# Performance work log

Hardware: AMD Instinct MI355X
Metric: run time of the kernel (lower is better)

## Reference

```python
import jax, jax.numpy as jnp
import numpy as np
from jax import lax

NFFT, WIN, HOP = 512, 320, 160
PAD = NFFT // 2
F = NFFT // 2 + 1  # 257

def _window():
    # torch.hann_window(320, periodic=True), center-padded to n_fft=512 (torch.stft convention)
    w = 0.5 - 0.5 * jnp.cos(2.0 * jnp.pi * jnp.arange(WIN, dtype=jnp.float32) / WIN)
    lp = (NFFT - WIN) // 2
    return jnp.pad(w, (lp, NFFT - WIN - lp))

def _stft(x):  # [N, L] -> [N, T, F] complex64 (center=True, reflect pad)
    xp = jnp.pad(x, ((0, 0), (PAD, PAD)), mode='reflect')
    T = 1 + (xp.shape[1] - NFFT) // HOP
    idx = jnp.arange(T)[:, None] * HOP + jnp.arange(NFFT)[None, :]
    frames = xp[:, idx] * _window()  # [N, T, NFFT]
    return jnp.fft.rfft(frames, axis=-1)

def _istft(spec, length):  # [N, T, F] complex -> [N, length]
    win = _window()
    frames = jnp.fft.irfft(spec, n=NFFT, axis=-1) * win  # [N, T, NFFT]
    N, T, _ = frames.shape
    total = (T - 1) * HOP + NFFT
    pos = (jnp.arange(T)[:, None] * HOP + jnp.arange(NFFT)[None, :]).reshape(-1)
    out = jnp.zeros((N, total), frames.dtype).at[:, pos].add(frames.reshape(N, -1))
    wsq = jnp.zeros((total,), win.dtype).at[pos].add(jnp.tile(win * win, T))
    out = out / jnp.maximum(wsq, 1e-11)[None, :]
    return out[:, PAD:PAD + length]

def _lstm(x, W_ih, W_hh, b_ih, b_hh):  # x [N, T, D] -> [N, T, H]
    N, T, _ = x.shape
    H = W_hh.shape[1]
    xW = x @ W_ih.T + (b_ih + b_hh)  # precompute input projections [N, T, 4H]
    def step(carry, xt):
        h, c = carry
        g = xt + h @ W_hh.T
        i, f, gg, o = jnp.split(g, 4, axis=-1)  # torch gate order i,f,g,o
        c = jax.nn.sigmoid(f) * c + jax.nn.sigmoid(i) * jnp.tanh(gg)
        h = jax.nn.sigmoid(o) * jnp.tanh(c)
        return (h, c), h
    h0 = jnp.zeros((N, H), x.dtype)
    _, hs = lax.scan(step, (h0, h0), jnp.swapaxes(xW, 0, 1))
    return jnp.swapaxes(hs, 0, 1)

def _forward(x, W_ih, W_hh, b_ih, b_hh, W1, b1, W2, b2):
    B, L, C = x.shape
    xm = jnp.transpose(x, (0, 2, 1)).reshape(B * C, L)
    spec = _stft(xm).reshape(B, C, -1, F)  # [B, C, T, F] == r_spec + 1j*i_spec
    T = spec.shape[2]
    feat = jnp.concatenate([spec.real, spec.imag], axis=-1).reshape(B * C, T, 2 * F)
    h = _lstm(feat, W_ih, W_hh, b_ih, b_hh)  # [B*C, T, 128]
    def masked(Wl, bl):
        m = h @ Wl.T + bl                      # [B*C, T, 514]
        rm, im = jnp.split(m, 2, axis=-1)
        mask = (rm + 1j * im).reshape(B, C, T, F)
        return mask * spec                      # complex mask multiply
    s_spec = masked(W1, b1)
    n_spec = masked(W2, b2)
    # per-frequency PSD matrices over time
    psd_s = jnp.einsum('bctf,betf->bfce', s_spec, jnp.conj(s_spec)) / T
    psd_n = jnp.einsum('bctf,betf->bfce', n_spec, jnp.conj(n_spec)) / T
    tr_n = jnp.einsum('bfcc->bf', psd_n).real
    eye = jnp.eye(C, dtype=psd_n.dtype)
    psd_n = psd_n + (1e-6 * tr_n / C + 1e-8)[..., None, None] * eye  # diagonal loading
    num = jnp.linalg.solve(psd_n, psd_s)                             # [B, F, C, C]
    ws = num / (jnp.einsum('bfcc->bf', num)[..., None, None] + 1e-8)
    w = ws[..., 0]                                                   # ref_channel = 0 -> [B, F, C]
    obs = jnp.transpose(spec, (0, 3, 1, 2))                          # [B, F, C, T]
    enh = jnp.einsum('bfc,bfct->bft', jnp.conj(w), obs)              # beamformed [B, F, T]
    return _istft(jnp.transpose(enh, (0, 2, 1)), L)                  # [B, L]

def setup_inputs() -> dict:
    key = jax.random.key(0)
    ks = jax.random.split(key, 8)
    D, H = 2 * F, 128
    s = 0.05
    return {
        'x': jax.random.normal(ks[0], (8, 96000, 8), jnp.float32),
        'W_ih': jax.random.normal(ks[1], (4 * H, D), jnp.float32) * s,
        'W_hh': jax.random.normal(ks[2], (4 * H, H), jnp.float32) * s,
        'b_ih': jnp.zeros((4 * H,), jnp.float32),
        'b_hh': jnp.zeros((4 * H,), jnp.float32),
        'W1': jax.random.normal(ks[3], (D, H), jnp.float32) * s,
        'b1': jnp.zeros((D,), jnp.float32),
        'W2': jax.random.normal(ks[4], (D, H), jnp.float32) * s,
        'b2': jnp.zeros((D,), jnp.float32),
    }

def reference(x, W_ih, W_hh, b_ih, b_hh, W1, b1, W2, b2):
    return _forward(x, W_ih, W_hh, b_ih, b_hh, W1, b1, W2, b2)
```

## Files before the change

### kernel.cpp

```cpp
#include <hip/hip_runtime.h>
#include <math.h>

#define NFFT  512
#define WINL  320
#define HOP   160
#define FPAD  256
#define NF    257
#define TT    601
#define LSEQ  96000
#define XPLEN 96512
#define NCH   8
#define NB    8
#define NSEQ  64
#define NROWS 38464
#define DD    514
#define HH    128
#define G4    512
#define KPAD  544
#define NCOMB 1026

#define NXP   24128
#define NWSQ  377
#define NBFF  1028
#define NWT   1088
#define NBI   1088
#define NBS   2
#define NWM   640
#define NWP   128
#define NINIT (NXP + NWSQ + NBFF + NWT + NBI + NBS + NWM + NWP)

typedef _Float16 h2v __attribute__((ext_vector_type(2)));
typedef short bf16x8 __attribute__((ext_vector_type(8)));
typedef float f32x4 __attribute__((ext_vector_type(4)));

__device__ __forceinline__ float winval(int k) {
  if (k < 96 || k >= 416) return 0.f;
  return 0.5f - 0.5f * cosf((float)(2.0 * M_PI / 320.0) * (float)(k - 96));
}

__device__ __forceinline__ void split_bf16(float v, unsigned short* h, unsigned short* l) {
  unsigned int hb = __float_as_uint(v) >> 16;
  float r = v - __uint_as_float(hb << 16);
  *h = (unsigned short)hb;
  *l = (unsigned short)(__float_as_uint(r) >> 16);
}

__device__ __forceinline__ void glds16(const unsigned short* g, unsigned short* l) {
  __builtin_amdgcn_global_load_lds(
      (const __attribute__((address_space(1))) void*)g,
      (__attribute__((address_space(3))) void*)l,
      16, 0, 0);
}

__device__ __forceinline__ int xcd_swz(int orig, int nwg) {
  int q = nwg >> 3, r = nwg & 7;
  int xcd = orig & 7, slot = orig >> 3;
  return (xcd < r ? xcd * (q + 1) : r * (q + 1) + (xcd - r) * q) + slot;
}

__global__ void k_init(const float* __restrict__ x, const float* __restrict__ Wih,
                       const float* __restrict__ Whh, const float* __restrict__ bih,
                       const float* __restrict__ bhh, const float* __restrict__ W1,
                       const float* __restrict__ W2,
                       unsigned short* __restrict__ XPh, unsigned short* __restrict__ XPl,
                       float* __restrict__ wsq, float* __restrict__ BFf,
                       unsigned short* __restrict__ WTh, unsigned short* __restrict__ WTl,
                       unsigned short* __restrict__ BIh, unsigned short* __restrict__ BIl,
                       float* __restrict__ BSUM,
                       unsigned short* __restrict__ W1h, unsigned short* __restrict__ W1l,
                       unsigned short* __restrict__ W2h, unsigned short* __restrict__ W2l,
                       unsigned int* __restrict__ WhhP4) {
  int b = blockIdx.x;
  const int tid = threadIdx.x;

  if (b < NXP) {
    int idx = b * 256 + tid;
    if (idx < NSEQ * XPLEN) {
      int n = idx / XPLEN, i = idx - n * XPLEN;
      int j = i - FPAD;
      if (j < 0) j = -j;
      else if (j >= LSEQ) j = 2 * LSEQ - 2 - j;
      int bb = n >> 3, c = n & 7;
      float v = x[((long)bb * LSEQ + j) * NCH + c];
      split_bf16(v, &XPh[idx], &XPl[idx]);
    }
    return;
  }
  b -= NXP;

  if (b < NWSQ) {
    int p = b * 256 + tid;
    if (p < XPLEN) {
      int t0 = (p <= 511) ? 0 : (p - 352) / 160;
      int t1 = p / 160; if (t1 > 600) t1 = 600;
      float s = 0.f;
      for (int t = t0; t <= t1; t++) { float w = winval(p - t * HOP); s += w * w; }
      wsq[p] = s;
    }
    return;
  }
  b -= NWSQ;

  if (b < NBFF) {
    int idx = b * 256 + tid;
    if (idx < NFFT * DD) {
      int k = idx / DD, d = idx - k * DD;
      float w = winval(k);
      int f = (d < NF) ? d : d - NF;
      int m = (k * f) & 511;
      float th = (float)(M_PI / 256.0) * (float)m;
      BFf[idx] = ((d < NF) ? cosf(th) : -sinf(th)) * w;
    }
    return;
  }
  b -= NBFF;

  if (b < NWT) {
    int idx = b * 256 + tid;
    if (idx < G4 * KPAD) {
      int n = idx / KPAD, k = idx - n * KPAD;
      float v = (k < DD) ? Wih[n * DD + k] : 0.f;
      split_bf16(v, &WTh[idx], &WTl[idx]);
    }
    return;
  }
  b -= NWT;

  if (b < NBI) {
    int idx = b * 256 + tid;
    if (idx < NFFT * KPAD) {
      int n = idx / KPAD, kk = idx - n * KPAD;
      float v = 0.f;
      if (kk < DD) {
        float w = winval(n);
        int f = (kk < NF) ? kk : kk - NF;
        int edge = (f == 0 || f == 256);
        float alpha = edge ? 1.f : 2.f;
        int m = (n * f) & 511;
        float th = (float)(M_PI / 256.0) * (float)m;
        float c;
        if (kk < NF) c = alpha * cosf(th);
        else         c = edge ? 0.f : -alpha * sinf(th);
        v = c * w * (1.f / 512.f);
      }
      split_bf16(v, &BIh[idx], &BIl[idx]);
    }
    return;
  }
  b -= NBI;

  if (b < NBS) {
    int idx = b * 256 + tid;
    if (idx < G4) BSUM[idx] = bih[idx] + bhh[idx];
    return;
  }
  b -= NBS;

  if (b < NWM) {
    int idx = b * 256 + tid;
    if (idx < 2 * 640 * HH) {
      int m = idx / (640 * HH);
      int rem = idx - m * 640 * HH;
      int np = rem / HH, k = rem - np * HH;
      int ri = np / 320, f = np - ri * 320;
      float v = 0.f;
      if (f < NF) {
        int fcol = (ri == 0) ? f : NF + f;
        v = (m == 0) ? W1[fcol * HH + k] : W2[fcol * HH + k];
      }
      unsigned short h, l;
      split_bf16(v, &h, &l);
      if (m == 0) { W1h[rem] = h; W1l[rem] = l; }
      else        { W2h[rem] = h; W2l[rem] = l; }
    }
    return;
  }
  b -= NWM;

  {
    int idx = b * 256 + tid;
    if (idx < G4 * 64) {
      int j = idx >> 6, k2 = idx & 63;
      _Float16 lo = (_Float16)Whh[j * HH + 2 * k2];
      _Float16 hi = (_Float16)Whh[j * HH + 2 * k2 + 1];
      unsigned int u = ((unsigned int)__builtin_bit_cast(unsigned short, hi) << 16)
                     |  (unsigned int)__builtin_bit_cast(unsigned short, lo);
      WhhP4[(k2 >> 2) * (G4 * 4) + j * 4 + (k2 & 3)] = u;
    }
  }
}

__global__ void k_bcomb(const float* __restrict__ BWf, unsigned short* __restrict__ H,
                        unsigned short* __restrict__ L) {
  int idx = blockIdx.x * 256 + threadIdx.x;
  if (idx >= 1152 * KPAD) return;
  int n = idx / KPAD, k = idx - n * KPAD;
  float v = 0.f;
  if (k < NFFT) {
    if (n < DD) {
      float w = winval(k);
      int f = (n < NF) ? n : n - NF;
      int m = (k * f) & 511;
      float th = (float)(M_PI / 256.0) * (float)m;
      v = ((n < NF) ? cosf(th) : -sinf(th)) * w;
    } else if (n < NCOMB) {
      v = BWf[k * G4 + (n - 514)];
    }
  }
  split_bf16(v, &H[idx], &L[idx]);
}

template <int GATHER>
__launch_bounds__(256)
__global__ void k_gemm3(const float* __restrict__ A,
                        const unsigned short* __restrict__ Bth,
                        const unsigned short* __restrict__ Btl,
                        const float* __restrict__ bias, float* __restrict__ C,
                        int M, int N, int K, int lda, int ldc) {
  __shared__ __align__(16) unsigned short sAh[128 * 40];
  __shared__ __align__(16) unsigned short sAl[128 * 40];
  __shared__ __align__(16) unsigned short sBh[128 * 40];
  __shared__ __align__(16) unsigned short sBl[128 * 40];
  const int tid = threadIdx.x;
  const int row0 = blockIdx.y * 128, col0 = blockIdx.x * 128;
  const int sar = tid >> 1, sak = (tid & 1) * 16;
  const int arow = row0 + sar;
  long abase = (long)arow * lda;
  const bool arok = (arow < M);
  const int lane = tid & 63, w = tid >> 6;
  const int wm = (w >> 1) * 64, wn = (w & 1) * 64;
  const int l15 = lane & 15, quad = lane >> 4;
  f32x4 acc[4][4] = {};
  unsigned int* aH = (unsigned int*)sAh;
  unsigned int* aL = (unsigned int*)sAl;
  uint4* bH = (uint4*)sBh;
  uint4* bL = (uint4*)sBl;
  for (int k0 = 0; k0 < K; k0 += 32) {
#pragma unroll
    for (int i = 0; i < 8; i++) {
      int kk = k0 + sak + 2 * i;
      float v0 = 0.f, v1 = 0.f;
      if (arok) {
        if (kk + 1 < K) { float2 t2 = *(const float2*)(A + abase + kk); v0 = t2.x; v1 = t2.y; }
        else if (kk < K) { v0 = A[abase + kk]; }
      }
      unsigned int h0 = __float_as_uint(v0) >> 16, h1 = __float_as_uint(v1) >> 16;
      float r0 = v0 - __uint_as_float(h0 << 16), r1 = v1 - __uint_as_float(h1 << 16);
      unsigned int l0 = __float_as_uint(r0) >> 16, l1 = __float_as_uint(r1) >> 16;
      aH[sar * 20 + (sak >> 1) + i] = h0 | (h1 << 16);
      aL[sar * 20 + (sak >> 1) + i] = l0 | (l1 << 16);
    }
#pragma unroll
    for (int h = 0; h < 2; h++) {
      int idx = tid + h * 256;
      int r = idx >> 2, c = idx & 3;
      long go = (long)(col0 + r) * KPAD + k0 + c * 8;
      bH[r * 5 + c] = *(const uint4*)(Bth + go);
      bL[r * 5 + c] = *(const uint4*)(Btl + go);
    }
    __syncthreads();
    bf16x8 ah[4], al[4], bh[4], bl[4];
#pragma unroll
    for (int i = 0; i < 4; i++) {
      int off = (wm + i * 16 + l15) * 40 + quad * 8;
      ah[i] = *(const bf16x8*)(sAh + off);
      al[i] = *(const bf16x8*)(sAl + off);
      int boff = (wn + i * 16 + l15) * 40 + quad * 8;
      bh[i] = *(const bf16x8*)(sBh + boff);
      bl[i] = *(const bf16x8*)(sBl + boff);
    }
#pragma unroll
    for (int i = 0; i < 4; i++)
#pragma unroll
      for (int j = 0; j < 4; j++) {
        acc[i][j] = __builtin_amdgcn_mfma_f32_16x16x32_bf16(al[i], bh[j], acc[i][j], 0, 0, 0);
        acc[i][j] = __builtin_amdgcn_mfma_f32_16x16x32_bf16(ah[i], bl[j], acc[i][j], 0, 0, 0);
        acc[i][j] = __builtin_amdgcn_mfma_f32_16x16x32_bf16(ah[i], bh[j], acc[i][j], 0, 0, 0);
      }
    __syncthreads();
  }
#pragma unroll
  for (int i = 0; i < 4; i++)
#pragma unroll
    for (int j = 0; j < 4; j++) {
      int cc = col0 + wn + j * 16 + l15;
      if (cc >= N) continue;
      float bv = bias ? bias[cc] : 0.f;
#pragma unroll
      for (int rg = 0; rg < 4; rg++) {
        int rr = row0 + wm + i * 16 + quad * 4 + rg;
        if (rr < M) C[(long)rr * ldc + cc] = acc[i][j][rg] + bv;
      }
    }
}

__launch_bounds__(256)
__global__ void k_gemm4(const unsigned short* __restrict__ Ah, const unsigned short* __restrict__ Al,
                        const unsigned short* __restrict__ Bh, const unsigned short* __restrict__ Bl,
                        const float* __restrict__ bsum, float* __restrict__ S,
                        float* __restrict__ XW) {
  __shared__ __align__(16) unsigned short sAh[128 * 32];
  __shared__ __align__(16) unsigned short sAl[128 * 32];
  __shared__ __align__(16) unsigned short sBh[128 * 32];
  __shared__ __align__(16) unsigned short sBl[128 * 32];
  const int tid = threadIdx.x;
  const int wg = xcd_swz(blockIdx.x, 9 * 301);
  const int row0 = (wg / 9) * 128, col0 = (wg % 9) * 128;
  const int lane = tid & 63, w = tid >> 6;
  const int wm = (w >> 1) * 64, wn = (w & 1) * 64;
  const int l15 = lane & 15, quad = lane >> 4;
  const int sr0 = w * 32 + (lane >> 2);
  const int sr1 = sr0 + 16;
  const int c8 = (lane & 3) * 8;
  long ab0, ab1;
  { int rr = row0 + sr0; int n = rr / TT, t = rr - n * TT; ab0 = (long)n * XPLEN + (long)t * HOP + c8; }
  { int rr = row0 + sr1; int n = rr / TT, t = rr - n * TT; ab1 = (long)n * XPLEN + (long)t * HOP + c8; }
  const long bb0 = (long)(col0 + sr0) * KPAD + c8;
  const long bb1 = (long)(col0 + sr1) * KPAD + c8;
  const int d0 = w * 1024;
  const int d1 = d0 + 512;
  f32x4 acc[4][4] = {};
  for (int k0 = 0; k0 < NFFT; k0 += 32) {
    glds16(Ah + ab0 + k0, sAh + d0);
    glds16(Ah + ab1 + k0, sAh + d1);
    glds16(Al + ab0 + k0, sAl + d0);
    glds16(Al + ab1 + k0, sAl + d1);
    glds16(Bh + bb0 + k0, sBh + d0);
    glds16(Bh + bb1 + k0, sBh + d1);
    glds16(Bl + bb0 + k0, sBl + d0);
    glds16(Bl + bb1 + k0, sBl + d1);
    __syncthreads();
    bf16x8 ah[4], al[4], bh[4], bl[4];
#pragma unroll
    for (int i = 0; i < 4; i++) {
      int off = (wm + i * 16 + l15) * 32 + quad * 8;
      ah[i] = *(const bf16x8*)(sAh + off);
      al[i] = *(const bf16x8*)(sAl + off);
      int boff = (wn + i * 16 + l15) * 32 + quad * 8;
      bh[i] = *(const bf16x8*)(sBh + boff);
      bl[i] = *(const bf16x8*)(sBl + boff);
    }
#pragma unroll
    for (int i = 0; i < 4; i++)
#pragma unroll
      for (int j = 0; j < 4; j++) {
        acc[i][j] = __builtin_amdgcn_mfma_f32_16x16x32_bf16(al[i], bh[j], acc[i][j], 0, 0, 0);
        acc[i][j] = __builtin_amdgcn_mfma_f32_16x16x32_bf16(ah[i], bl[j], acc[i][j], 0, 0, 0);
        acc[i][j] = __builtin_amdgcn_mfma_f32_16x16x32_bf16(ah[i], bh[j], acc[i][j], 0, 0, 0);
      }
    __syncthreads();
  }
#pragma unroll
  for (int i = 0; i < 4; i++)
#pragma unroll
    for (int j = 0; j < 4; j++) {
      int cc = col0 + wn + j * 16 + l15;
      if (cc >= NCOMB) continue;
#pragma unroll
      for (int rg = 0; rg < 4; rg++) {
        int rr = row0 + wm + i * 16 + quad * 4 + rg;
        if (rr >= NROWS) continue;
        float v = acc[i][j][rg];
        if (cc < DD) S[(long)rr * DD + cc] = v;
        else         XW[(long)rr * G4 + (cc - 514)] = v + bsum[cc - 514];
      }
    }
}

__launch_bounds__(256)
__global__ void k_gemm5(const unsigned short* __restrict__ Ah, const unsigned short* __restrict__ Al,
                        const unsigned short* __restrict__ Bh, const unsigned short* __restrict__ Bl,
                        float* __restrict__ C, int M, int N, int ldc) {
  __shared__ __align__(16) unsigned short sAh[128 * 40];
  __shared__ __align__(16) unsigned short sAl[128 * 40];
  __shared__ __align__(16) unsigned short sBh[128 * 40];
  __shared__ __align__(16) unsigned short sBl[128 * 40];
  const int tid = threadIdx.x;
  const int row0 = blockIdx.y * 128, col0 = blockIdx.x * 128;
  const int sr0 = tid >> 2, c4 = (tid & 3) * 8, cq = tid & 3;
  const int lane = tid & 63, w = tid >> 6;
  const int wm = (w >> 1) * 64, wn = (w & 1) * 64;
  const int l15 = lane & 15, quad = lane >> 4;
  f32x4 acc[4][4] = {};
  uint4* aH4 = (uint4*)sAh; uint4* aL4 = (uint4*)sAl;
  uint4* bH4 = (uint4*)sBh; uint4* bL4 = (uint4*)sBl;
  for (int k0 = 0; k0 < KPAD; k0 += 32) {
    {
      long go = (long)(row0 + sr0) * KPAD + k0 + c4;
      aH4[sr0 * 5 + cq] = *(const uint4*)(Ah + go);
      aL4[sr0 * 5 + cq] = *(const uint4*)(Al + go);
      go = (long)(row0 + sr0 + 64) * KPAD + k0 + c4;
      aH4[(sr0 + 64) * 5 + cq] = *(const uint4*)(Ah + go);
      aL4[(sr0 + 64) * 5 + cq] = *(const uint4*)(Al + go);
    }
    {
      long go = (long)(col0 + sr0) * KPAD + k0 + c4;
      bH4[sr0 * 5 + cq] = *(const uint4*)(Bh + go);
      bL4[sr0 * 5 + cq] = *(const uint4*)(Bl + go);
      go = (long)(col0 + sr0 + 64) * KPAD + k0 + c4;
      bH4[(sr0 + 64) * 5 + cq] = *(const uint4*)(Bh + go);
      bL4[(sr0 + 64) * 5 + cq] = *(const uint4*)(Bl + go);
    }
    __syncthreads();
    bf16x8 ah[4], al[4], bh[4], bl[4];
#pragma unroll
    for (int i = 0; i < 4; i++) {
      int off = (wm + i * 16 + l15) * 40 + quad * 8;
      ah[i] = *(const bf16x8*)(sAh + off);
      al[i] = *(const bf16x8*)(sAl + off);
      int boff = (wn + i * 16 + l15) * 40 + quad * 8;
      bh[i] = *(const bf16x8*)(sBh + boff);
      bl[i] = *(const bf16x8*)(sBl + boff);
    }
#pragma unroll
    for (int i = 0; i < 4; i++)
#pragma unroll
      for (int j = 0; j < 4; j++) {
        acc[i][j] = __builtin_amdgcn_mfma_f32_16x16x32_bf16(al[i], bh[j], acc[i][j], 0, 0, 0);
        acc[i][j] = __builtin_amdgcn_mfma_f32_16x16x32_bf16(ah[i], bl[j], acc[i][j], 0, 0, 0);
        acc[i][j] = __builtin_amdgcn_mfma_f32_16x16x32_bf16(ah[i], bh[j], acc[i][j], 0, 0, 0);
      }
    __syncthreads();
  }
#pragma unroll
  for (int i = 0; i < 4; i++)
#pragma unroll
    for (int j = 0; j < 4; j++) {
      int cc = col0 + wn + j * 16 + l15;
      if (cc >= N) continue;
#pragma unroll
      for (int rg = 0; rg < 4; rg++) {
        int rr = row0 + wm + i * 16 + quad * 4 + rg;
        if (rr < M) C[(long)rr * ldc + cc] = acc[i][j][rg];
      }
    }
}

__device__ __forceinline__ float tanh_fast(float x) {
  float e = __expf(2.f * x);
  return 1.f - 2.f / (e + 1.f);
}

__launch_bounds__(512, 2)
__global__ void k_lstm(const float* __restrict__ XW, const unsigned int* __restrict__ WhhP4,
                       float* __restrict__ Hout) {
  __shared__ __align__(16) unsigned int hl2[64];
  __shared__ float gl[G4];
  const int j = threadIdx.x;
  const int n = blockIdx.x;
  const uint4* W4 = (const uint4*)WhhP4;
  unsigned int wp[64];
#pragma unroll
  for (int i4 = 0; i4 < 16; i4++) {
    uint4 v = W4[i4 * G4 + j];
    wp[4 * i4]     = v.x;
    wp[4 * i4 + 1] = v.y;
    wp[4 * i4 + 2] = v.z;
    wp[4 * i4 + 3] = v.w;
  }
  float cst = 0.f;
  if (j < 64) hl2[j] = 0u;
  const float* xwrow = XW + (long)n * TT * G4 + j;
  float xnext = xwrow[0];
  const uint4* h4 = (const uint4*)hl2;
  const bool isg = (j >= 2 * HH) && (j < 3 * HH);
  __syncthreads();
  for (int t = 0; t < TT; t++) {
    float xv = xnext;
    if (t + 1 < TT) xnext = xwrow[(long)(t + 1) * G4];
    float a0 = 0.f, a1 = 0.f, a2 = 0.f, a3 = 0.f;
#pragma unroll
    for (int k = 0; k < 16; k++) {
      uint4 hv4 = h4[k];
      a0 = __builtin_amdgcn_fdot2(__builtin_bit_cast(h2v, hv4.x), __builtin_bit_cast(h2v, wp[4 * k]),     a0, false);
      a1 = __builtin_amdgcn_fdot2(__builtin_bit_cast(h2v, hv4.y), __builtin_bit_cast(h2v, wp[4 * k + 1]), a1, false);
      a2 = __builtin_amdgcn_fdot2(__builtin_bit_cast(h2v, hv4.z), __builtin_bit_cast(h2v, wp[4 * k + 2]), a2, false);
      a3 = __builtin_amdgcn_fdot2(__builtin_bit_cast(h2v, hv4.w), __builtin_bit_cast(h2v, wp[4 * k + 3]), a3, false);
    }
    float a = ((a0 + a1) + (a2 + a3)) + xv;
    float nl;
    if (isg) nl = tanh_fast(a);
    else     nl = 1.f / (1.f + __expf(-a));
    gl[j] = nl;
    asm volatile("s_waitcnt lgkmcnt(0)" ::: "memory");
    __builtin_amdgcn_s_barrier();
    if (j < HH) {
      float ni = gl[j], nf = gl[HH + j], ng = gl[2 * HH + j], no = gl[3 * HH + j];
      cst = nf * cst + ni * ng;
      float hv = no * tanh_fast(cst);
      ((_Float16*)hl2)[j] = (_Float16)hv;
      Hout[((long)n * TT + t) * HH + j] = hv;
    }
    asm volatile("s_waitcnt lgkmcnt(0)" ::: "memory");
    __builtin_amdgcn_s_barrier();
  }
}

__launch_bounds__(256)
__global__ void k_maskms(const float* __restrict__ Hout,
                         const unsigned short* __restrict__ Wsh,
                         const unsigned short* __restrict__ Wsl,
                         const float* __restrict__ bias, const float* __restrict__ S,
                         float* __restrict__ MS) {
  __shared__ __align__(16) unsigned short sAh[64 * 40];
  __shared__ __align__(16) unsigned short sAl[64 * 40];
  __shared__ __align__(16) unsigned short sBh[64 * 40];
  __shared__ __align__(16) unsigned short sBl[64 * 40];
  __shared__ float Cs[64][68];
  __shared__ float SR[64][33];
  __shared__ float SI[64][33];
  const int tid = threadIdx.x;
  const int wg = xcd_swz(blockIdx.x, 9 * 601);
  const int f0 = (wg % 9) * 32;
  const int row0 = (wg / 9) * 64;
  const int lane = tid & 63, w = tid >> 6;
  const int wm = w * 16;
  const int l15 = lane & 15, quad = lane >> 4;
  const int sar = tid >> 2;
  const int sak = (tid & 3) * 8;
  const int np = ((sar < 32) ? 0 : 320 - 32) + f0 + sar;
  unsigned int* aH = (unsigned int*)sAh;
  unsigned int* aL = (unsigned int*)sAl;
  f32x4 acc[4] = {};
  for (int k0 = 0; k0 < HH; k0 += 32) {
    {
      const float* ap = Hout + (long)(row0 + sar) * HH + k0 + sak;
      float4 v0 = *(const float4*)ap;
      float4 v1 = *(const float4*)(ap + 4);
      float vv[8] = {v0.x, v0.y, v0.z, v0.w, v1.x, v1.y, v1.z, v1.w};
#pragma unroll
      for (int i = 0; i < 4; i++) {
        unsigned int h0 = __float_as_uint(vv[2 * i]) >> 16, h1 = __float_as_uint(vv[2 * i + 1]) >> 16;
        float r0 = vv[2 * i] - __uint_as_float(h0 << 16), r1 = vv[2 * i + 1] - __uint_as_float(h1 << 16);
        unsigned int l0 = __float_as_uint(r0) >> 16, l1 = __float_as_uint(r1) >> 16;
        aH[sar * 20 + (sak >> 1) + i] = h0 | (h1 << 16);
        aL[sar * 20 + (sak >> 1) + i] = l0 | (l1 << 16);
      }
    }
    {
      long go = (long)np * HH + k0 + sak;
      *(uint4*)(sBh + sar * 40 + sak) = *(const uint4*)(Wsh + go);
      *(uint4*)(sBl + sar * 40 + sak) = *(const uint4*)(Wsl + go);
    }
    __syncthreads();
    bf16x8 ah = *(const bf16x8*)(sAh + (wm + l15) * 40 + quad * 8);
    bf16x8 al = *(const bf16x8*)(sAl + (wm + l15) * 40 + quad * 8);
#pragma unroll
    for (int ct = 0; ct < 4; ct++) {
      bf16x8 bh = *(const bf16x8*)(sBh + (ct * 16 + l15) * 40 + quad * 8);
      bf16x8 bl = *(const bf16x8*)(sBl + (ct * 16 + l15) * 40 + quad * 8);
      acc[ct] = __builtin_amdgcn_mfma_f32_16x16x32_bf16(al, bh, acc[ct], 0, 0, 0);
      acc[ct] = __builtin_amdgcn_mfma_f32_16x16x32_bf16(ah, bl, acc[ct], 0, 0, 0);
      acc[ct] = __builtin_amdgcn_mfma_f32_16x16x32_bf16(ah, bh, acc[ct], 0, 0, 0);
    }
    __syncthreads();
  }
#pragma unroll
  for (int ct = 0; ct < 4; ct++) {
    int col = ct * 16 + l15;
    int f = f0 + (col & 31);
    int fcol = (col < 32) ? f : NF + f;
    float bv = (f < NF) ? bias[fcol] : 0.f;
#pragma unroll
    for (int rg = 0; rg < 4; rg++) Cs[wm + quad * 4 + rg][col] = acc[ct][rg] + bv;
  }
  __syncthreads();
  {
    int fl = tid & 31, r8 = tid >> 5;
    int f = f0 + fl;
#pragma unroll
    for (int i = 0; i < 8; i++) {
      int rl = r8 * 8 + i;
      int rr = row0 + rl;
      float rm = Cs[rl][fl], im = Cs[rl][32 + fl];
      float sr = 0.f, si = 0.f;
      if (f < NF) { sr = S[(long)rr * DD + f]; si = S[(long)rr * DD + NF + f]; }
      SR[rl][fl] = rm * sr - im * si;
      SI[rl][fl] = rm * si + im * sr;
    }
  }
  __syncthreads();
  {
    int tl = tid & 63, fq = tid >> 6;
    int rr = row0 + tl;
    int n = rr / TT, t = rr - n * TT;
    int b = n >> 3, c = n & 7;
#pragma unroll
    for (int i = 0; i < 8; i++) {
      int fl = fq * 8 + i;
      int f = f0 + fl;
      if (f < NF) {
        long addr = ((((long)b * NF + f) * 8 + c) * (long)TT + t) * 2;
        *(float2*)&MS[addr] = make_float2(SR[tl][fl], SI[tl][fl]);
      }
    }
  }
}

__launch_bounds__(256)
__global__ void k_psd(const float* __restrict__ MS, float* __restrict__ PSD) {
  __shared__ float buf[9616];
  __shared__ float part[64][8];
  const int tid = threadIdx.x;
  const long base = (long)blockIdx.x * 9616;
  for (int i = tid; i < 9616; i += 256) buf[i] = MS[base + i];
  __syncthreads();
  int p = tid & 63, q = tid >> 6;
  int c = p >> 3, e = p & 7;
  const float2* xc = (const float2*)&buf[c * 1202];
  const float2* xe = (const float2*)&buf[e * 1202];
  int t0 = q * 150, t1 = (q == 3) ? TT : t0 + 150;
  float ar = 0.f, ai = 0.f;
  for (int t = t0; t < t1; t++) {
    float2 m = xc[t];
    float2 v = xe[t];
    ar += m.x * v.x + m.y * v.y;
    ai += m.y * v.x - m.x * v.y;
  }
  part[p][q * 2] = ar; part[p][q * 2 + 1] = ai;
  __syncthreads();
  if (tid < 64) {
    float sr = part[tid][0] + part[tid][2] + part[tid][4] + part[tid][6];
    float si = part[tid][1] + part[tid][3] + part[tid][5] + part[tid][7];
    PSD[((long)blockIdx.x * 64 + tid) * 2]     = sr * (1.f / 601.f);
    PSD[((long)blockIdx.x * 64 + tid) * 2 + 1] = si * (1.f / 601.f);
  }
}

__launch_bounds__(64)
__global__ void k_solve(const float* __restrict__ PS, const float* __restrict__ PN,
                        float* __restrict__ WV) {
  int idx = blockIdx.x * 64 + threadIdx.x;
  if (idx >= NB * NF) return;
  float Ar[8][8], Ai[8][8], Br[8][8], Bi[8][8];
  const float* pn = PN + (long)idx * 128;
  const float* ps = PS + (long)idx * 128;
  for (int i = 0; i < 8; i++)
    for (int j = 0; j < 8; j++) {
      Ar[i][j] = pn[(i * 8 + j) * 2]; Ai[i][j] = pn[(i * 8 + j) * 2 + 1];
      Br[i][j] = ps[(i * 8 + j) * 2]; Bi[i][j] = ps[(i * 8 + j) * 2 + 1];
    }
  float tr = 0.f;
  for (int i = 0; i < 8; i++) tr += Ar[i][i];
  float load = 1e-6f * tr / 8.f + 1e-8f;
  for (int i = 0; i < 8; i++) Ar[i][i] += load;
  for (int k = 0; k < 8; k++) {
    int piv = k; float mx = Ar[k][k] * Ar[k][k] + Ai[k][k] * Ai[k][k];
    for (int i = k + 1; i < 8; i++) {
      float m2 = Ar[i][k] * Ar[i][k] + Ai[i][k] * Ai[i][k];
      if (m2 > mx) { mx = m2; piv = i; }
    }
    if (piv != k) {
      for (int j = 0; j < 8; j++) {
        float t0;
        t0 = Ar[k][j]; Ar[k][j] = Ar[piv][j]; Ar[piv][j] = t0;
        t0 = Ai[k][j]; Ai[k][j] = Ai[piv][j]; Ai[piv][j] = t0;
        t0 = Br[k][j]; Br[k][j] = Br[piv][j]; Br[piv][j] = t0;
        t0 = Bi[k][j]; Bi[k][j] = Bi[piv][j]; Bi[piv][j] = t0;
      }
    }
    float dr = Ar[k][k], di = Ai[k][k];
    float inv = 1.f / (dr * dr + di * di);
    float irr = dr * inv, iii = -di * inv;
    for (int j = 0; j < 8; j++) {
      float xr = Ar[k][j], xi = Ai[k][j];
      Ar[k][j] = xr * irr - xi * iii; Ai[k][j] = xr * iii + xi * irr;
      xr = Br[k][j]; xi = Bi[k][j];
      Br[k][j] = xr * irr - xi * iii; Bi[k][j] = xr * iii + xi * irr;
    }
    for (int i = 0; i < 8; i++) {
      if (i == k) continue;
      float fr = Ar[i][k], fi = Ai[i][k];
      for (int j = 0; j < 8; j++) {
        float kr = Ar[k][j], ki = Ai[k][j];
        Ar[i][j] -= fr * kr - fi * ki;
        Ai[i][j] -= fr * ki + fi * kr;
        kr = Br[k][j]; ki = Bi[k][j];
        Br[i][j] -= fr * kr - fi * ki;
        Bi[i][j] -= fr * ki + fi * kr;
      }
    }
  }
  float trr = 1e-8f, tri = 0.f;
  for (int i = 0; i < 8; i++) { trr += Br[i][i]; tri += Bi[i][i]; }
  float inv = 1.f / (trr * trr + tri * tri);
  for (int c = 0; c < 8; c++) {
    float xr = Br[c][0], xi = Bi[c][0];
    WV[((long)idx * 8 + c) * 2]     = (xr * trr + xi * tri) * inv;
    WV[((long)idx * 8 + c) * 2 + 1] = (xi * trr - xr * tri) * inv;
  }
}

__launch_bounds__(320)
__global__ void k_beam(const float* __restrict__ S, const float* __restrict__ WV,
                       unsigned short* __restrict__ ENHh, unsigned short* __restrict__ ENHl) {
  __shared__ float WL[NF * 16];
  int bb = blockIdx.x / TT, t = blockIdx.x - bb * TT;
  for (int i = threadIdx.x; i < NF * 16; i += 320) WL[i] = WV[(long)bb * NF * 16 + i];
  __syncthreads();
  int f = threadIdx.x;
  long base = ((long)bb * TT + t) * KPAD;
  if (f < NF) {
    float er = 0.f, ei = 0.f;
#pragma unroll
    for (int c = 0; c < 8; c++) {
      float wr = WL[(f * 8 + c) * 2], wi = WL[(f * 8 + c) * 2 + 1];
      const float* srow = S + (((long)(bb * 8 + c) * TT) + t) * DD;
      float sr = srow[f], si = srow[NF + f];
      er += wr * sr + wi * si;
      ei += wr * si - wi * sr;
    }
    split_bf16(er, &ENHh[base + f], &ENHl[base + f]);
    split_bf16(ei, &ENHh[base + NF + f], &ENHl[base + NF + f]);
  }
  int z = threadIdx.x - 288;
  if (z >= 0 && z < 30) { ENHh[base + DD + z] = 0; ENHl[base + DD + z] = 0; }
}

__global__ void k_ola(const float* __restrict__ IFR, const float* __restrict__ WSQ,
                      float* __restrict__ out) {
  int idx = blockIdx.x * 256 + threadIdx.x;
  if (idx >= NB * LSEQ) return;
  int b = idx / LSEQ, l = idx - b * LSEQ;
  int p = l + FPAD;
  int t0 = (p <= 511) ? 0 : (p - 352) / 160;
  int t1 = p / 160; if (t1 > 600) t1 = 600;
  float s = 0.f;
  for (int t = t0; t <= t1; t++) s += IFR[((long)b * TT + t) * NFFT + (p - t * HOP)];
  out[idx] = s / fmaxf(WSQ[p], 1e-11f);
}

extern "C" void kernel_launch(void* const* d_in, const int* in_sizes, int n_in,
                              void* d_out, int out_size, void* d_ws, size_t ws_size,
                              hipStream_t stream) {
  (void)in_sizes; (void)n_in; (void)out_size; (void)ws_size;
  const float* x   = (const float*)d_in[0];
  const float* Wih = (const float*)d_in[1];
  const float* Whh = (const float*)d_in[2];
  const float* bih = (const float*)d_in[3];
  const float* bhh = (const float*)d_in[4];
  const float* W1  = (const float*)d_in[5];
  const float* b1  = (const float*)d_in[6];
  const float* W2  = (const float*)d_in[7];
  const float* b2  = (const float*)d_in[8];
  float* ws = (float*)d_ws;

  unsigned short* XPh = (unsigned short*)(ws + 0);
  unsigned short* XPl = (unsigned short*)(ws + 3088384);
  float* S     = ws + 6176768;
  float* XWM   = ws + 25951264;
  float* HOUT  = ws + 45725760;
  float* PSD_S = ws + 50650048;
  float* PSD_N = ws + 50913216;
  float* WV    = ws + 51176384;
  float* BSUM  = ws + 51209280;
  float* WSQ   = ws + 51209792;
  unsigned short* W1sh = (unsigned short*)(ws + 51306304);
  unsigned short* W1sl = (unsigned short*)(ws + 51347264);
  unsigned short* W2sh = (unsigned short*)(ws + 51388224);
  unsigned short* W2sl = (unsigned short*)(ws + 51429184);
  unsigned short* WTth = (unsigned short*)(ws + 51470144);
  unsigned short* WTtl = (unsigned short*)(ws + 51609408);
  unsigned short* BIth = (unsigned short*)(ws + 51748672);
  unsigned short* BItl = (unsigned short*)(ws + 51887936);
  float* MS    = XWM;
  float* IFR   = ws + 0;
  unsigned int* WhhP4 = (unsigned int*)(XWM + 19693568);
  float* BFf = HOUT;
  float* BWf = HOUT + 263168;
  unsigned short* BCh = (unsigned short*)(HOUT + 525312);
  unsigned short* BCl = (unsigned short*)(HOUT + 838656);
  unsigned short* ENHh = (unsigned short*)HOUT;
  unsigned short* ENHl = (unsigned short*)(HOUT + 1307776);

  k_init<<<NINIT, 256, 0, stream>>>(x, Wih, Whh, bih, bhh, W1, W2,
                                    XPh, XPl, WSQ, BFf, WTth, WTtl, BIth, BItl,
                                    BSUM, W1sh, W1sl, W2sh, W2sl, WhhP4);

  {
    dim3 g(4, 4);
    k_gemm3<0><<<g, 256, 0, stream>>>(BFf, WTth, WTtl, nullptr, BWf, 512, 512, DD, DD, G4);
  }
  k_bcomb<<<(1152 * KPAD + 255) / 256, 256, 0, stream>>>(BWf, BCh, BCl);

  k_gemm4<<<9 * 301, 256, 0, stream>>>(XPh, XPl, BCh, BCl, BSUM, S, XWM);

  k_lstm<<<64, 512, 0, stream>>>(XWM, WhhP4, HOUT);

  k_maskms<<<9 * 601, 256, 0, stream>>>(HOUT, W1sh, W1sl, b1, S, MS);
  k_psd<<<NB * NF, 256, 0, stream>>>(MS, PSD_S);
  k_maskms<<<9 * 601, 256, 0, stream>>>(HOUT, W2sh, W2sl, b2, S, MS);
  k_psd<<<NB * NF, 256, 0, stream>>>(MS, PSD_N);

  k_solve<<<(NB * NF + 63) / 64, 64, 0, stream>>>(PSD_S, PSD_N, WV);
  k_beam<<<NB * TT, 320, 0, stream>>>(S, WV, ENHh, ENHl);

  {
    dim3 g(4, 38);
    k_gemm5<<<g, 256, 0, stream>>>(ENHh, ENHl, BIth, BItl, IFR, NB * TT, NFFT, NFFT);
  }

  k_ola<<<(NB * LSEQ + 255) / 256, 256, 0, stream>>>(IFR, WSQ, (float*)d_out);
}
```

Baseline: 1.088 ms.

## Overlap part of the STFT GEMM with the LSTM recurrence in one launch

The column tiles 0-3 of the combined STFT+input-projection GEMM, which hold only spectrum columns not needed by the LSTM, are moved out of the first GEMM launch. They are computed by extra blocks of a fused LSTM kernel, so the 64 latency-bound LSTM blocks no longer leave most CUs idle. The LSTM blocks raise their wave priority so they are not starved. This costs an extra copy of the bf16 DFT basis into scratch buffers, and the GEMM blocks run at 512 threads with half of them idle, which may hurt occupancy or contend with the LSTM blocks.

```diff
diff --git a/kernel.cpp b/kernel.cpp
--- a/kernel.cpp
+++ b/kernel.cpp
@@ -191,7 +191,8 @@
 }
 
 __global__ void k_bcomb(const float* __restrict__ BWf, unsigned short* __restrict__ H,
-                        unsigned short* __restrict__ L) {
+                        unsigned short* __restrict__ L,
+                        unsigned short* __restrict__ BFsh, unsigned short* __restrict__ BFsl) {
   int idx = blockIdx.x * 256 + threadIdx.x;
   if (idx >= 1152 * KPAD) return;
   int n = idx / KPAD, k = idx - n * KPAD;
@@ -207,7 +208,10 @@
       v = BWf[k * G4 + (n - 514)];
     }
   }
-  split_bf16(v, &H[idx], &L[idx]);
+  unsigned short h, l;
+  split_bf16(v, &h, &l);
+  H[idx] = h; L[idx] = l;
+  if (n < 512) { BFsh[idx] = h; BFsl[idx] = l; }
 }
 
 template <int GATHER>
@@ -298,14 +302,14 @@
 __global__ void k_gemm4(const unsigned short* __restrict__ Ah, const unsigned short* __restrict__ Al,
                         const unsigned short* __restrict__ Bh, const unsigned short* __restrict__ Bl,
                         const float* __restrict__ bsum, float* __restrict__ S,
-                        float* __restrict__ XW) {
+                        float* __restrict__ XW, int colBase, int nCT) {
   __shared__ __align__(16) unsigned short sAh[128 * 32];
   __shared__ __align__(16) unsigned short sAl[128 * 32];
   __shared__ __align__(16) unsigned short sBh[128 * 32];
   __shared__ __align__(16) unsigned short sBl[128 * 32];
   const int tid = threadIdx.x;
-  const int wg = xcd_swz(blockIdx.x, 9 * 301);
-  const int row0 = (wg / 9) * 128, col0 = (wg % 9) * 128;
+  const int wg = xcd_swz(blockIdx.x, nCT * 301);
+  const int row0 = (wg / nCT) * 128, col0 = (colBase + wg % nCT) * 128;
   const int lane = tid & 63, w = tid >> 6;
   const int wm = (w >> 1) * 64, wn = (w & 1) * 64;
   const int l15 = lane & 15, quad = lane >> 4;
@@ -441,58 +445,139 @@
   return 1.f - 2.f / (e + 1.f);
 }
 
-__launch_bounds__(512, 2)
-__global__ void k_lstm(const float* __restrict__ XW, const unsigned int* __restrict__ WhhP4,
-                       float* __restrict__ Hout) {
+__launch_bounds__(512)
+__global__ void k_lstm_s(const float* __restrict__ XW, const unsigned int* __restrict__ WhhP4,
+                         float* __restrict__ Hout,
+                         const unsigned short* __restrict__ Ah, const unsigned short* __restrict__ Al,
+                         const unsigned short* __restrict__ Bh, const unsigned short* __restrict__ Bl,
+                         float* __restrict__ S) {
+  __shared__ __align__(16) unsigned short sAh[128 * 32];
+  __shared__ __align__(16) unsigned short sAl[128 * 32];
+  __shared__ __align__(16) unsigned short sBh[128 * 32];
+  __shared__ __align__(16) unsigned short sBl[128 * 32];
   __shared__ __align__(16) unsigned int hl2[64];
   __shared__ float gl[G4];
-  const int j = threadIdx.x;
-  const int n = blockIdx.x;
-  const uint4* W4 = (const uint4*)WhhP4;
-  unsigned int wp[64];
-#pragma unroll
-  for (int i4 = 0; i4 < 16; i4++) {
-    uint4 v = W4[i4 * G4 + j];
-    wp[4 * i4]     = v.x;
-    wp[4 * i4 + 1] = v.y;
-    wp[4 * i4 + 2] = v.z;
-    wp[4 * i4 + 3] = v.w;
-  }
-  float cst = 0.f;
-  if (j < 64) hl2[j] = 0u;
-  const float* xwrow = XW + (long)n * TT * G4 + j;
-  float xnext = xwrow[0];
-  const uint4* h4 = (const uint4*)hl2;
-  const bool isg = (j >= 2 * HH) && (j < 3 * HH);
-  __syncthreads();
-  for (int t = 0; t < TT; t++) {
-    float xv = xnext;
-    if (t + 1 < TT) xnext = xwrow[(long)(t + 1) * G4];
-    float a0 = 0.f, a1 = 0.f, a2 = 0.f, a3 = 0.f;
-#pragma unroll
-    for (int k = 0; k < 16; k++) {
-      uint4 hv4 = h4[k];
-      a0 = __builtin_amdgcn_fdot2(__builtin_bit_cast(h2v, hv4.x), __builtin_bit_cast(h2v, wp[4 * k]),     a0, false);
-      a1 = __builtin_amdgcn_fdot2(__builtin_bit_cast(h2v, hv4.y), __builtin_bit_cast(h2v, wp[4 * k + 1]), a1, false);
-      a2 = __builtin_amdgcn_fdot2(__builtin_bit_cast(h2v, hv4.z), __builtin_bit_cast(h2v, wp[4 * k + 2]), a2, false);
-      a3 = __builtin_amdgcn_fdot2(__builtin_bit_cast(h2v, hv4.w), __builtin_bit_cast(h2v, wp[4 * k + 3]), a3, false);
-    }
-    float a = ((a0 + a1) + (a2 + a3)) + xv;
-    float nl;
-    if (isg) nl = tanh_fast(a);
-    else     nl = 1.f / (1.f + __expf(-a));
-    gl[j] = nl;
-    asm volatile("s_waitcnt lgkmcnt(0)" ::: "memory");
-    __builtin_amdgcn_s_barrier();
-    if (j < HH) {
-      float ni = gl[j], nf = gl[HH + j], ng = gl[2 * HH + j], no = gl[3 * HH + j];
-      cst = nf * cst + ni * ng;
-      float hv = no * tanh_fast(cst);
-      ((_Float16*)hl2)[j] = (_Float16)hv;
-      Hout[((long)n * TT + t) * HH + j] = hv;
-    }
-    asm volatile("s_waitcnt lgkmcnt(0)" ::: "memory");
-    __builtin_amdgcn_s_barrier();
+  const int tid = threadIdx.x;
+
+  if (blockIdx.x < 64) {
+    __builtin_amdgcn_s_setprio(1);
+    const int j = tid;
+    const int n = blockIdx.x;
+    const uint4* W4 = (const uint4*)WhhP4;
+    unsigned int wp[64];
+#pragma unroll
+    for (int i4 = 0; i4 < 16; i4++) {
+      uint4 v = W4[i4 * G4 + j];
+      wp[4 * i4]     = v.x;
+      wp[4 * i4 + 1] = v.y;
+      wp[4 * i4 + 2] = v.z;
+      wp[4 * i4 + 3] = v.w;
+    }
+    float cst = 0.f;
+    if (j < 64) hl2[j] = 0u;
+    const float* xwrow = XW + (long)n * TT * G4 + j;
+    float xnext = xwrow[0];
+    const uint4* h4 = (const uint4*)hl2;
+    const bool isg = (j >= 2 * HH) && (j < 3 * HH);
+    __syncthreads();
+    for (int t = 0; t < TT; t++) {
+      float xv = xnext;
+      if (t + 1 < TT) xnext = xwrow[(long)(t + 1) * G4];
+      float a0 = 0.f, a1 = 0.f, a2 = 0.f, a3 = 0.f;
+#pragma unroll
+      for (int k = 0; k < 16; k++) {
+        uint4 hv4 = h4[k];
+        a0 = __builtin_amdgcn_fdot2(__builtin_bit_cast(h2v, hv4.x), __builtin_bit_cast(h2v, wp[4 * k]),     a0, false);
+        a1 = __builtin_amdgcn_fdot2(__builtin_bit_cast(h2v, hv4.y), __builtin_bit_cast(h2v, wp[4 * k + 1]), a1, false);
+        a2 = __builtin_amdgcn_fdot2(__builtin_bit_cast(h2v, hv4.z), __builtin_bit_cast(h2v, wp[4 * k + 2]), a2, false);
+        a3 = __builtin_amdgcn_fdot2(__builtin_bit_cast(h2v, hv4.w), __builtin_bit_cast(h2v, wp[4 * k + 3]), a3, false);
+      }
+      float a = ((a0 + a1) + (a2 + a3)) + xv;
+      float nl;
+      if (isg) nl = tanh_fast(a);
+      else     nl = 1.f / (1.f + __expf(-a));
+      gl[j] = nl;
+      asm volatile("s_waitcnt lgkmcnt(0)" ::: "memory");
+      __builtin_amdgcn_s_barrier();
+      if (j < HH) {
+        float ni = gl[j], nf = gl[HH + j], ng = gl[2 * HH + j], no = gl[3 * HH + j];
+        cst = nf * cst + ni * ng;
+        float hv = no * tanh_fast(cst);
+        ((_Float16*)hl2)[j] = (_Float16)hv;
+        Hout[((long)n * TT + t) * HH + j] = hv;
+      }
+      asm volatile("s_waitcnt lgkmcnt(0)" ::: "memory");
+      __builtin_amdgcn_s_barrier();
+    }
+    __builtin_amdgcn_s_setprio(0);
+    return;
+  }
+
+  const int wg = xcd_swz(blockIdx.x - 64, 4 * 301);
+  const int row0 = (wg >> 2) * 128, col0 = (wg & 3) * 128;
+  const int lane = tid & 63, w = tid >> 6;
+  const int wm = (w >> 1) * 64, wn = (w & 1) * 64;
+  const int l15 = lane & 15, quad = lane >> 4;
+  const int sr0 = w * 32 + (lane >> 2);
+  const int sr1 = sr0 + 16;
+  const int c8 = (lane & 3) * 8;
+  long ab0 = 0, ab1 = 0, bb0 = 0, bb1 = 0;
+  int d0 = 0, d1 = 0;
+  if (tid < 256) {
+    { int rr = row0 + sr0; int n = rr / TT, t = rr - n * TT; ab0 = (long)n * XPLEN + (long)t * HOP + c8; }
+    { int rr = row0 + sr1; int n = rr / TT, t = rr - n * TT; ab1 = (long)n * XPLEN + (long)t * HOP + c8; }
+    bb0 = (long)(col0 + sr0) * KPAD + c8;
+    bb1 = (long)(col0 + sr1) * KPAD + c8;
+    d0 = w * 1024;
+    d1 = d0 + 512;
+  }
+  f32x4 acc[4][4] = {};
+  for (int k0 = 0; k0 < NFFT; k0 += 32) {
+    if (tid < 256) {
+      glds16(Ah + ab0 + k0, sAh + d0);
+      glds16(Ah + ab1 + k0, sAh + d1);
+      glds16(Al + ab0 + k0, sAl + d0);
+      glds16(Al + ab1 + k0, sAl + d1);
+      glds16(Bh + bb0 + k0, sBh + d0);
+      glds16(Bh + bb1 + k0, sBh + d1);
+      glds16(Bl + bb0 + k0, sBl + d0);
+      glds16(Bl + bb1 + k0, sBl + d1);
+    }
+    __syncthreads();
+    if (tid < 256) {
+      bf16x8 ah[4], al[4], bh[4], bl[4];
+#pragma unroll
+      for (int i = 0; i < 4; i++) {
+        int off = (wm + i * 16 + l15) * 32 + quad * 8;
+        ah[i] = *(const bf16x8*)(sAh + off);
+        al[i] = *(const bf16x8*)(sAl + off);
+        int boff = (wn + i * 16 + l15) * 32 + quad * 8;
+        bh[i] = *(const bf16x8*)(sBh + boff);
+        bl[i] = *(const bf16x8*)(sBl + boff);
+      }
+#pragma unroll
+      for (int i = 0; i < 4; i++)
+#pragma unroll
+        for (int j = 0; j < 4; j++) {
+          acc[i][j] = __builtin_amdgcn_mfma_f32_16x16x32_bf16(al[i], bh[j], acc[i][j], 0, 0, 0);
+          acc[i][j] = __builtin_amdgcn_mfma_f32_16x16x32_bf16(ah[i], bl[j], acc[i][j], 0, 0, 0);
+          acc[i][j] = __builtin_amdgcn_mfma_f32_16x16x32_bf16(ah[i], bh[j], acc[i][j], 0, 0, 0);
+        }
+    }
+    __syncthreads();
+  }
+  if (tid < 256) {
+#pragma unroll
+    for (int i = 0; i < 4; i++)
+#pragma unroll
+      for (int j = 0; j < 4; j++) {
+        int cc = col0 + wn + j * 16 + l15;
+#pragma unroll
+        for (int rg = 0; rg < 4; rg++) {
+          int rr = row0 + wm + i * 16 + quad * 4 + rg;
+          if (rr < NROWS) S[(long)rr * DD + cc] = acc[i][j][rg];
+        }
+      }
   }
 }
 
@@ -770,6 +855,8 @@
   float* BWf = HOUT + 263168;
   unsigned short* BCh = (unsigned short*)(HOUT + 525312);
   unsigned short* BCl = (unsigned short*)(HOUT + 838656);
+  unsigned short* BFsh = (unsigned short*)PSD_S;
+  unsigned short* BFsl = (unsigned short*)PSD_N;
   unsigned short* ENHh = (unsigned short*)HOUT;
   unsigned short* ENHl = (unsigned short*)(HOUT + 1307776);
 
@@ -781,11 +868,11 @@
     dim3 g(4, 4);
     k_gemm3<0><<<g, 256, 0, stream>>>(BFf, WTth, WTtl, nullptr, BWf, 512, 512, DD, DD, G4);
   }
-  k_bcomb<<<(1152 * KPAD + 255) / 256, 256, 0, stream>>>(BWf, BCh, BCl);
-
-  k_gemm4<<<9 * 301, 256, 0, stream>>>(XPh, XPl, BCh, BCl, BSUM, S, XWM);
-
-  k_lstm<<<64, 512, 0, stream>>>(XWM, WhhP4, HOUT);
+  k_bcomb<<<(1152 * KPAD + 255) / 256, 256, 0, stream>>>(BWf, BCh, BCl, BFsh, BFsl);
+
+  k_gemm4<<<5 * 301, 256, 0, stream>>>(XPh, XPl, BCh, BCl, BSUM, S, XWM, 4, 5);
+
+  k_lstm_s<<<64 + 4 * 301, 512, 0, stream>>>(XWM, WhhP4, HOUT, XPh, XPl, BFsh, BFsl, S);
 
   k_maskms<<<9 * 601, 256, 0, stream>>>(HOUT, W1sh, W1sl, b1, S, MS);
   k_psd<<<NB * NF, 256, 0, stream>>>(MS, PSD_S);
```

Measured after the change: 1.021 ms. 6.2% less time.
